# Performance work log

Measured on AMD Instinct MI355X. Metric: run time of the kernel, lower is better.

Reference implementation:

```python
import jax, jax.numpy as jnp
import numpy as np

OUT_FEATURES = 4096
IN_FEATURES = 4096
NNZ = 1677722
BATCH, SEQ = 2, 2048


def setup_inputs() -> dict:
    key = jax.random.key(0)
    k1, k2, k3, k4 = jax.random.split(key, 4)
    x = jax.random.normal(k1, (BATCH, SEQ, IN_FEATURES), dtype=jnp.float32)
    data = jax.random.normal(k2, (NNZ,), dtype=jnp.float32)
    rows = jax.random.randint(k3, (NNZ,), 0, OUT_FEATURES, dtype=jnp.int32)
    cols = jax.random.randint(k4, (NNZ,), 0, IN_FEATURES, dtype=jnp.int32)
    return {"x": x, "data": data, "rows": rows, "cols": cols}


def reference(x, data, rows, cols):
    # Densify sparse weight W [out_features, in_features] from COO triples
    # (equivalent math to the CSR spmm in the original module).
    W = jnp.zeros((OUT_FEATURES, IN_FEATURES), dtype=data.dtype)
    W = W.at[rows, cols].add(data)
    # Original: (W @ x_flat.T).T reshaped -> y = x @ W^T, shape [B, S, out]
    return jnp.einsum("bsi,oi->bso", x, W)
```

## Files before the change

kernel.cpp:

```cpp
#include <hip/hip_runtime.h>
#include <stdint.h>

#define M_ROWS 4096
#define N_OUT  4096
#define K_IN   4096
#define NNZ_N  1677722

typedef __attribute__((ext_vector_type(8))) short  bf16x8_t;
typedef __attribute__((ext_vector_type(4))) float  f32x4_t;

__device__ __forceinline__ unsigned short f2bf(float f) {
    union { float f; uint32_t u; } v; v.f = f;
    uint32_t u = v.u;
    u += 0x7FFFu + ((u >> 16) & 1u);
    return (unsigned short)(u >> 16);
}

__global__ void zero_and_convert_x(uint4* __restrict__ Wz,
                                   const float4* __restrict__ x,
                                   uint4* __restrict__ xo) {
    int i = blockIdx.x * blockDim.x + threadIdx.x;
    uint4 z; z.x = z.y = z.z = z.w = 0u;
    Wz[i] = z;
    float4 a = x[2 * i], b = x[2 * i + 1];
    uint4 o;
    o.x = (uint32_t)f2bf(a.x) | ((uint32_t)f2bf(a.y) << 16);
    o.y = (uint32_t)f2bf(a.z) | ((uint32_t)f2bf(a.w) << 16);
    o.z = (uint32_t)f2bf(b.x) | ((uint32_t)f2bf(b.y) << 16);
    o.w = (uint32_t)f2bf(b.z) | ((uint32_t)f2bf(b.w) << 16);
    xo[i] = o;
}

__global__ void scatter_coo_bf16(const float* __restrict__ data,
                                 const int* __restrict__ rows,
                                 const int* __restrict__ cols,
                                 unsigned short* __restrict__ W, int nnz) {
    int i = blockIdx.x * blockDim.x + threadIdx.x;
    if (i < nnz) {
        size_t idx = (size_t)rows[i] * K_IN + cols[i];
        uint32_t hv = (uint32_t)f2bf(data[i]);
        uint32_t pk = (idx & 1) ? (hv << 16) : hv;
        uint32_t* addr = (uint32_t*)(W + (idx & ~(size_t)1));
        asm volatile("global_atomic_pk_add_bf16 %0, %1, off"
                     :: "v"(addr), "v"(pk) : "memory");
    }
}

__device__ __forceinline__ void async_ld16(const void* g, void* lds_wave_base) {
    __builtin_amdgcn_global_load_lds(
        (const __attribute__((address_space(1))) uint32_t*)g,
        (__attribute__((address_space(3))) uint32_t*)lds_wave_base,
        16, 0, 0);
}

#define STAGE_M(gbase, lbase, kt, slot) do {                                   \
    const unsigned short* g_ = (gbase) + (kt) * 64;                            \
    unsigned short*       l_ = (lbase) + (slot) * 32768;                       \
    async_ld16(g_,                  l_);                                       \
    async_ld16(g_ + 1 * 64 * K_IN,  l_ + 4096);                                \
    async_ld16(g_ + 2 * 64 * K_IN,  l_ + 8192);                                \
    async_ld16(g_ + 3 * 64 * K_IN,  l_ + 12288);                               \
} while (0)

__global__ __launch_bounds__(512, 2) void gemm_bt(const unsigned short* __restrict__ A,
                                                  const unsigned short* __restrict__ B,
                                                  float* __restrict__ C) {
    __shared__ __align__(16) unsigned short lds_[65536];

    const int t    = threadIdx.x;
    const int wave = t >> 6;
    const int lane = t & 63;
    const int wr   = wave >> 2;
    const int wc   = wave & 3;
    const int m0   = blockIdx.y * 256;
    const int n0   = blockIdx.x * 256;

    const int srow = t >> 3;
    const int sch  = ((t & 7) ^ (srow & 7)) * 8;
    const unsigned short* gA = A + (size_t)(m0 + srow) * K_IN + sch;
    const unsigned short* gB = B + (size_t)(n0 + srow) * K_IN + sch;
    unsigned short* lA = lds_ + wave * 512;
    unsigned short* lB = lds_ + 16384 + wave * 512;

    const int l15  = lane & 15;
    const int aoff = (wr * 128 + l15) * 64;
    const int boff = (wc * 64  + l15) * 64;
    const int ck0  = (((lane >> 4)    ) ^ (lane & 7)) * 8;
    const int ck1  = (((lane >> 4) | 4) ^ (lane & 7)) * 8;

    f32x4_t acc[8][4];
#pragma unroll
    for (int i = 0; i < 8; ++i)
#pragma unroll
        for (int j = 0; j < 4; ++j) acc[i][j] = (f32x4_t){0.f, 0.f, 0.f, 0.f};

    bf16x8_t af[4][2], bf0[2][2], bf1[2][2];

    STAGE_M(gA, lA, 0, 0); STAGE_M(gB, lB, 0, 0);
    STAGE_M(gA, lA, 1, 1); STAGE_M(gB, lB, 1, 1);
    asm volatile("s_waitcnt vmcnt(8)" ::: "memory");
    __builtin_amdgcn_s_barrier();

    for (int kt = 0; kt < 64; ++kt) {
        const unsigned short* pA = lds_ + (kt & 1) * 32768;
        const unsigned short* pB = pA + 16384;

#pragma unroll
        for (int im = 0; im < 4; ++im) {
            af[im][0] = *(const bf16x8_t*)(pA + aoff + im * 1024 + ck0);
            af[im][1] = *(const bf16x8_t*)(pA + aoff + im * 1024 + ck1);
        }
#pragma unroll
        for (int jn = 0; jn < 2; ++jn) {
            bf0[jn][0] = *(const bf16x8_t*)(pB + boff + jn * 1024 + ck0);
            bf0[jn][1] = *(const bf16x8_t*)(pB + boff + jn * 1024 + ck1);
        }
        __builtin_amdgcn_s_barrier();
        asm volatile("s_waitcnt lgkmcnt(0)" ::: "memory");
        __builtin_amdgcn_s_setprio(1);
#pragma unroll
        for (int im = 0; im < 4; ++im)
#pragma unroll
            for (int jn = 0; jn < 2; ++jn)
#pragma unroll
                for (int kk = 0; kk < 2; ++kk)
                    acc[im][jn] = __builtin_amdgcn_mfma_f32_16x16x32_bf16(
                        af[im][kk], bf0[jn][kk], acc[im][jn], 0, 0, 0);
        __builtin_amdgcn_s_setprio(0);
        __builtin_amdgcn_s_barrier();

#pragma unroll
        for (int jn = 0; jn < 2; ++jn) {
            bf1[jn][0] = *(const bf16x8_t*)(pB + boff + (2 + jn) * 1024 + ck0);
            bf1[jn][1] = *(const bf16x8_t*)(pB + boff + (2 + jn) * 1024 + ck1);
        }
        __builtin_amdgcn_s_barrier();
        asm volatile("s_waitcnt lgkmcnt(0)" ::: "memory");
        __builtin_amdgcn_s_setprio(1);
#pragma unroll
        for (int im = 0; im < 4; ++im)
#pragma unroll
            for (int jn = 0; jn < 2; ++jn)
#pragma unroll
                for (int kk = 0; kk < 2; ++kk)
                    acc[im][2 + jn] = __builtin_amdgcn_mfma_f32_16x16x32_bf16(
                        af[im][kk], bf1[jn][kk], acc[im][2 + jn], 0, 0, 0);
        __builtin_amdgcn_s_setprio(0);
        __builtin_amdgcn_s_barrier();

        if (kt < 62) STAGE_M(gB, lB, kt + 2, (kt & 1));
#pragma unroll
        for (int im = 0; im < 4; ++im) {
            af[im][0] = *(const bf16x8_t*)(pA + aoff + (4 + im) * 1024 + ck0);
            af[im][1] = *(const bf16x8_t*)(pA + aoff + (4 + im) * 1024 + ck1);
        }
        __builtin_amdgcn_s_barrier();
        asm volatile("s_waitcnt lgkmcnt(0)" ::: "memory");
        __builtin_amdgcn_s_setprio(1);
#pragma unroll
        for (int im = 0; im < 4; ++im)
#pragma unroll
            for (int jn = 0; jn < 2; ++jn)
#pragma unroll
                for (int kk = 0; kk < 2; ++kk)
                    acc[4 + im][jn] = __builtin_amdgcn_mfma_f32_16x16x32_bf16(
                        af[im][kk], bf0[jn][kk], acc[4 + im][jn], 0, 0, 0);
        __builtin_amdgcn_s_setprio(0);
        __builtin_amdgcn_s_barrier();

        if (kt < 62) STAGE_M(gA, lA, kt + 2, (kt & 1));
        __builtin_amdgcn_s_setprio(1);
#pragma unroll
        for (int im = 0; im < 4; ++im)
#pragma unroll
            for (int jn = 0; jn < 2; ++jn)
#pragma unroll
                for (int kk = 0; kk < 2; ++kk)
                    acc[4 + im][2 + jn] = __builtin_amdgcn_mfma_f32_16x16x32_bf16(
                        af[im][kk], bf1[jn][kk], acc[4 + im][2 + jn], 0, 0, 0);
        __builtin_amdgcn_s_setprio(0);
        if (kt < 62) {
            asm volatile("s_waitcnt vmcnt(8)" ::: "memory");
        } else {
            asm volatile("s_waitcnt vmcnt(0)" ::: "memory");
        }
        __builtin_amdgcn_s_barrier();
    }

    const int crow = m0 + wr * 128 + ((lane >> 4) << 2);
    const int ccol = n0 + wc * 64 + l15;
#pragma unroll
    for (int im = 0; im < 8; ++im)
#pragma unroll
        for (int jn = 0; jn < 4; ++jn)
#pragma unroll
            for (int r = 0; r < 4; ++r)
                C[(size_t)(crow + im * 16 + r) * N_OUT + ccol + jn * 16] =
                    acc[im][jn][r];
}

extern "C" void kernel_launch(void* const* d_in, const int* in_sizes, int n_in,
                              void* d_out, int out_size, void* d_ws, size_t ws_size,
                              hipStream_t stream) {
    const float* x    = (const float*)d_in[0];
    const float* data = (const float*)d_in[1];
    const int*   rows = (const int*)d_in[2];
    const int*   cols = (const int*)d_in[3];
    float*       out  = (float*)d_out;

    unsigned short* W_bf16 = (unsigned short*)d_ws;
    unsigned short* x_bf16 = (unsigned short*)((char*)d_ws + (32u << 20));

    zero_and_convert_x<<<(N_OUT * K_IN) / (8 * 256), 256, 0, stream>>>(
        (uint4*)W_bf16, (const float4*)x, (uint4*)x_bf16);

    scatter_coo_bf16<<<(NNZ_N + 255) / 256, 256, 0, stream>>>(
        data, rows, cols, W_bf16, NNZ_N);

    dim3 grid(N_OUT / 256, M_ROWS / 256);
    gemm_bt<<<grid, 512, 0, stream>>>(x_bf16, W_bf16, out);
}
```

Measured before the change: 323.0 us.

## Densify COO via per-row binning and LDS fp32 accumulation instead of global bf16 atomics

```diff
diff --git a/kernel.cpp b/kernel.cpp
--- a/kernel.cpp
+++ b/kernel.cpp
@@ -5,6 +5,7 @@
 #define N_OUT  4096
 #define K_IN   4096
 #define NNZ_N  1677722
+#define CAP    640
 
 typedef __attribute__((ext_vector_type(8))) short  bf16x8_t;
 typedef __attribute__((ext_vector_type(4))) float  f32x4_t;
@@ -16,12 +17,14 @@
     return (unsigned short)(u >> 16);
 }
 
-__global__ void zero_and_convert_x(uint4* __restrict__ Wz,
-                                   const float4* __restrict__ x,
-                                   uint4* __restrict__ xo) {
+__global__ void convert_x_zero_cnt(const float4* __restrict__ x,
+                                   uint4* __restrict__ xo,
+                                   uint4* __restrict__ cntz) {
     int i = blockIdx.x * blockDim.x + threadIdx.x;
-    uint4 z; z.x = z.y = z.z = z.w = 0u;
-    Wz[i] = z;
+    if (i < 16384) {
+        uint4 z; z.x = z.y = z.z = z.w = 0u;
+        cntz[i] = z;
+    }
     float4 a = x[2 * i], b = x[2 * i + 1];
     uint4 o;
     o.x = (uint32_t)f2bf(a.x) | ((uint32_t)f2bf(a.y) << 16);
@@ -31,18 +34,52 @@
     xo[i] = o;
 }
 
-__global__ void scatter_coo_bf16(const float* __restrict__ data,
-                                 const int* __restrict__ rows,
-                                 const int* __restrict__ cols,
-                                 unsigned short* __restrict__ W, int nnz) {
+__global__ void bin_coo(const float* __restrict__ data,
+                        const int* __restrict__ rows,
+                        const int* __restrict__ cols,
+                        uint32_t* __restrict__ cnt,
+                        uint32_t* __restrict__ bucket, int nnz) {
     int i = blockIdx.x * blockDim.x + threadIdx.x;
-    if (i < nnz) {
-        size_t idx = (size_t)rows[i] * K_IN + cols[i];
-        uint32_t hv = (uint32_t)f2bf(data[i]);
-        uint32_t pk = (idx & 1) ? (hv << 16) : hv;
-        uint32_t* addr = (uint32_t*)(W + (idx & ~(size_t)1));
-        asm volatile("global_atomic_pk_add_bf16 %0, %1, off"
-                     :: "v"(addr), "v"(pk) : "memory");
+    if (i >= nnz) return;
+    int r = rows[i];
+    uint32_t slot = atomicAdd(&cnt[r << 4], 1u);
+    if (slot < CAP)
+        bucket[(size_t)r * CAP + slot] =
+            ((uint32_t)cols[i] << 16) | (uint32_t)f2bf(data[i]);
+}
+
+__global__ __launch_bounds__(256) void accum_rows(const uint32_t* __restrict__ cnt,
+                                                  const uint32_t* __restrict__ bucket,
+                                                  unsigned short* __restrict__ W) {
+    __shared__ float acc[K_IN];
+    const int r = blockIdx.x;
+    const int t = threadIdx.x;
+
+    float4* av = (float4*)acc;
+#pragma unroll
+    for (int j = t; j < K_IN / 4; j += 256) av[j] = (float4){0.f, 0.f, 0.f, 0.f};
+    __syncthreads();
+
+    uint32_t n = cnt[r << 4];
+    if (n > CAP) n = CAP;
+    const uint32_t* b = bucket + (size_t)r * CAP;
+    for (uint32_t j = t; j < n; j += 256) {
+        uint32_t e = b[j];
+        union { uint32_t u; float f; } v; v.u = (e & 0xFFFFu) << 16;
+        atomicAdd(&acc[e >> 16], v.f);
+    }
+    __syncthreads();
+
+    uint4* wv = (uint4*)(W + (size_t)r * K_IN);
+#pragma unroll
+    for (int j = t; j < K_IN / 8; j += 256) {
+        float4 a = av[2 * j], c = av[2 * j + 1];
+        uint4 o;
+        o.x = (uint32_t)f2bf(a.x) | ((uint32_t)f2bf(a.y) << 16);
+        o.y = (uint32_t)f2bf(a.z) | ((uint32_t)f2bf(a.w) << 16);
+        o.z = (uint32_t)f2bf(c.x) | ((uint32_t)f2bf(c.y) << 16);
+        o.w = (uint32_t)f2bf(c.z) | ((uint32_t)f2bf(c.w) << 16);
+        wv[j] = o;
     }
 }
 
@@ -210,12 +247,16 @@
 
     unsigned short* W_bf16 = (unsigned short*)d_ws;
     unsigned short* x_bf16 = (unsigned short*)((char*)d_ws + (32u << 20));
-
-    zero_and_convert_x<<<(N_OUT * K_IN) / (8 * 256), 256, 0, stream>>>(
-        (uint4*)W_bf16, (const float4*)x, (uint4*)x_bf16);
-
-    scatter_coo_bf16<<<(NNZ_N + 255) / 256, 256, 0, stream>>>(
-        data, rows, cols, W_bf16, NNZ_N);
+    uint32_t*       cnt    = (uint32_t*)((char*)d_ws + (64u << 20));
+    uint32_t*       bucket = (uint32_t*)((char*)d_ws + (65u << 20));
+
+    convert_x_zero_cnt<<<(M_ROWS * K_IN) / (8 * 256), 256, 0, stream>>>(
+        (const float4*)x, (uint4*)x_bf16, (uint4*)cnt);
+
+    bin_coo<<<(NNZ_N + 255) / 256, 256, 0, stream>>>(
+        data, rows, cols, cnt, bucket, NNZ_N);
+
+    accum_rows<<<N_OUT, 256, 0, stream>>>(cnt, bucket, W_bf16);
 
     dim3 grid(N_OUT / 256, M_ROWS / 256);
     gemm_bt<<<grid, 512, 0, stream>>>(x_bf16, W_bf16, out);
```

Measured after the change: 338.2 us. 1.05x slower.
